# Kernel optimization log

Measured on AMD Instinct MI355X. Metric: run time of the kernel, lower is better.

Reference implementation:

```python
import jax, jax.numpy as jnp
import numpy as np

B, N, E, H, NE = 8, 512, 512, 8, 16384
DH = E // H
SCALE = DH ** -0.5
EPS = 1e-5


def _layernorm(x, g, b):
    mu = jnp.mean(x, axis=-1, keepdims=True)
    var = jnp.var(x, axis=-1, keepdims=True)
    return (x - mu) / jnp.sqrt(var + EPS) * g + b


def setup_inputs() -> dict:
    key = jax.random.key(0)
    ks = jax.random.split(key, 24)
    s = 0.02
    return {
        "x": jax.random.normal(ks[0], (B, N, E), jnp.float32),
        "edge_attr": jax.random.normal(ks[1], (NE, E), jnp.float32),
        "Wq": jax.random.normal(ks[2], (E, E), jnp.float32) * s,
        "bq": jnp.zeros((E,), jnp.float32),
        "Wk": jax.random.normal(ks[3], (E, E), jnp.float32) * s,
        "bk": jnp.zeros((E,), jnp.float32),
        "Wv": jax.random.normal(ks[4], (E, E), jnp.float32) * s,
        "bv": jnp.zeros((E,), jnp.float32),
        "Wo": jax.random.normal(ks[5], (E, E), jnp.float32) * s,
        "bo": jnp.zeros((E,), jnp.float32),
        "dist_table": jax.random.normal(ks[6], (100, H), jnp.float32),
        "We": jax.random.normal(ks[7], (H, E), jnp.float32) * s,
        "be": jnp.zeros((H,), jnp.float32),
        "W1": jax.random.normal(ks[8], (4 * E, E), jnp.float32) * s,
        "b1": jnp.zeros((4 * E,), jnp.float32),
        "W2": jax.random.normal(ks[9], (E, 4 * E), jnp.float32) * s,
        "b2": jnp.zeros((E,), jnp.float32),
        "g1": jnp.ones((E,), jnp.float32),
        "beta1": jnp.zeros((E,), jnp.float32),
        "g2": jnp.ones((E,), jnp.float32),
        "beta2": jnp.zeros((E,), jnp.float32),
        "edge_index": jax.random.randint(ks[10], (2, NE), 0, N, jnp.int64),
        "distance_matrix": jax.random.randint(ks[11], (B, N, N), 0, 100, jnp.int32),
    }


def reference(x, edge_attr, Wq, bq, Wk, bk, Wv, bv, Wo, bo, dist_table, We, be,
              W1, b1, W2, b2, g1, beta1, g2, beta2, edge_index, distance_matrix):
    residual = x
    h = _layernorm(x, g1, beta1)
    # projections -> [B, H, N, DH]
    def proj(W, b):
        return (h @ W.T + b).reshape(B, N, H, DH).transpose(0, 2, 1, 3)
    q, k, v = proj(Wq, bq), proj(Wk, bk), proj(Wv, bv)
    attn = jnp.einsum('bhnd,bhmd->bhnm', q, k) * SCALE
    # distance-encoding gather: [B,N,N] -> [B,N,N,H] -> [B,H,N,N]
    d_idx = jnp.clip(distance_matrix, 0, 99)
    attn = attn + dist_table[d_idx].transpose(0, 3, 1, 2)
    # per-edge scatter-add bias (duplicates accumulate, matching sequential loop)
    edge_enc = (edge_attr @ We.T + be).T  # [H, NE]
    src, tgt = edge_index[0], edge_index[1]
    edge_bias = jnp.zeros((H, N, N), attn.dtype).at[:, src, tgt].add(edge_enc)
    attn = attn + edge_bias[None]
    attn = jax.nn.softmax(attn, axis=-1)
    out = jnp.einsum('bhnm,bhmd->bhnd', attn, v)
    out = out.transpose(0, 2, 1, 3).reshape(B, N, E)
    out = out @ Wo.T + bo
    x1 = residual + out
    h2 = _layernorm(x1, g2, beta2)
    ffn = jax.nn.gelu(h2 @ W1.T + b1, approximate=False) @ W2.T + b2
    return x1 + ffn
```

## Files before the change

kernel.cpp:

```cpp
#include <hip/hip_runtime.h>
#include <cstdint>
#include <cstddef>

#define B_  8
#define N_  512
#define E_  512
#define H_  8
#define DH_ 64
#define NE_ 16384
#define QT  64

using u16   = unsigned short;
using bf16x8 = __attribute__((ext_vector_type(8))) __bf16;
using u16x8  = __attribute__((ext_vector_type(8))) unsigned short;
using f32x4  = __attribute__((ext_vector_type(4))) float;

__device__ __forceinline__ u16 f2b(float f) {
  unsigned u = __builtin_bit_cast(unsigned, f);
  u += 0x7fffu + ((u >> 16) & 1u);
  return (u16)(u >> 16);
}

__device__ __forceinline__ bf16x8 ld_frag(const u16* p) {
  return __builtin_bit_cast(bf16x8, *(const u16x8*)p);
}

__device__ __forceinline__ void gemm_core_128x128(
    const u16* __restrict__ At, int lda,
    const u16* __restrict__ Bt, int ldb, int K,
    u16* ldsA, u16* ldsB, f32x4 (&acc)[4][4]) {
  const int tid  = threadIdx.x;
  const int wid  = tid >> 6, lane = tid & 63;
  const int wr   = wid >> 1, wc = wid & 1;
  const int qd   = lane >> 4, r = lane & 15;
  const int mrow = tid >> 2, k0 = (tid & 3) * 8;
  for (int kt = 0; kt < K; kt += 32) {
    __syncthreads();
    *(u16x8*)&ldsA[mrow*32 + k0]      = *(const u16x8*)&At[(size_t)mrow*lda + kt + k0];
    *(u16x8*)&ldsA[(mrow+64)*32 + k0] = *(const u16x8*)&At[(size_t)(mrow+64)*lda + kt + k0];
    *(u16x8*)&ldsB[mrow*32 + k0]      = *(const u16x8*)&Bt[(size_t)mrow*ldb + kt + k0];
    *(u16x8*)&ldsB[(mrow+64)*32 + k0] = *(const u16x8*)&Bt[(size_t)(mrow+64)*ldb + kt + k0];
    __syncthreads();
    bf16x8 af[4], bfv[4];
#pragma unroll
    for (int i = 0; i < 4; ++i) af[i] = ld_frag(&ldsA[(wr*64 + i*16 + r)*32 + qd*8]);
#pragma unroll
    for (int j = 0; j < 4; ++j) bfv[j] = ld_frag(&ldsB[(wc*64 + j*16 + r)*32 + qd*8]);
#pragma unroll
    for (int i = 0; i < 4; ++i)
#pragma unroll
      for (int j = 0; j < 4; ++j)
        acc[i][j] = __builtin_amdgcn_mfma_f32_16x16x32_bf16(af[i], bfv[j], acc[i][j], 0, 0, 0);
  }
}

template <int EPI>
__global__ __launch_bounds__(256) void gemm_epi(
    const u16* __restrict__ A, const u16* __restrict__ W,
    const float* __restrict__ bias, const float* __restrict__ res,
    float* __restrict__ outf, u16* __restrict__ outb, int Kd, int Nd) {
  __shared__ u16 ldsA[128*32];
  __shared__ u16 ldsB[128*32];
  const int bx = blockIdx.x, by = blockIdx.y;
  f32x4 acc[4][4] = {};
  gemm_core_128x128(A + (size_t)bx*128*Kd, Kd, W + (size_t)by*128*Kd, Kd, Kd,
                    ldsA, ldsB, acc);
  const int tid = threadIdx.x, wid = tid>>6, lane = tid&63;
  const int wr = wid>>1, wc = wid&1, qd = lane>>4, r = lane&15;
#pragma unroll
  for (int i = 0; i < 4; ++i) {
#pragma unroll
    for (int j = 0; j < 4; ++j) {
      const int grow = bx*128 + wr*64 + i*16 + qd*4;
      const int gcol = by*128 + wc*64 + j*16 + r;
      const float bb = bias[gcol];
#pragma unroll
      for (int rg = 0; rg < 4; ++rg) {
        float v = acc[i][j][rg] + bb;
        const size_t idx = (size_t)(grow + rg)*Nd + gcol;
        if constexpr (EPI == 0) {
          outb[idx] = f2b(v);
        } else if constexpr (EPI == 1) {
          outf[idx] = v + res[idx];
        } else {
          v = 0.5f * v * (1.0f + erff(v * 0.70710678118f));
          outb[idx] = f2b(v);
        }
      }
    }
  }
}

__global__ __launch_bounds__(256) void qkv_gemm_k(
    const u16* __restrict__ A,
    const u16* __restrict__ Wqb, const u16* __restrict__ Wkb, const u16* __restrict__ Wvb,
    const float* __restrict__ bq, const float* __restrict__ bk, const float* __restrict__ bv,
    u16* __restrict__ qo, u16* __restrict__ ko, u16* __restrict__ vo) {
  __shared__ u16 ldsA[128*32];
  __shared__ u16 ldsB[128*32];
  const int bx = blockIdx.x, by = blockIdx.y, z = blockIdx.z;
  const u16*   W    = z == 0 ? Wqb : (z == 1 ? Wkb : Wvb);
  const float* bias = z == 0 ? bq  : (z == 1 ? bk  : bv);
  u16*         outb = z == 0 ? qo  : (z == 1 ? ko  : vo);
  f32x4 acc[4][4] = {};
  gemm_core_128x128(A + (size_t)bx*128*E_, E_, W + (size_t)by*128*E_, E_, E_,
                    ldsA, ldsB, acc);
  const int tid = threadIdx.x, wid = tid>>6, lane = tid&63;
  const int wr = wid>>1, wc = wid&1, qd = lane>>4, r = lane&15;
#pragma unroll
  for (int i = 0; i < 4; ++i) {
#pragma unroll
    for (int j = 0; j < 4; ++j) {
      const int grow = bx*128 + wr*64 + i*16 + qd*4;
      const int gcol = by*128 + wc*64 + j*16 + r;
      const float bb = bias[gcol];
#pragma unroll
      for (int rg = 0; rg < 4; ++rg)
        outb[(size_t)(grow + rg)*E_ + gcol] = f2b(acc[i][j][rg] + bb);
    }
  }
}

__global__ __launch_bounds__(256) void flash_attn_k(
    const u16* __restrict__ qm, const u16* __restrict__ km, const u16* __restrict__ vm,
    const float* __restrict__ dtab, const int* __restrict__ Dm,
    const float* __restrict__ ebias, u16* __restrict__ outb) {
  __shared__ u16 sQ[QT*72];
  __shared__ u16 sK[128*72];
  __shared__ u16 sP[QT*136];
  __shared__ u16 sVt[64*136];
  __shared__ float sDtab[100*H_];
  __shared__ float sMax[2][QT], sSum[2][QT], sM[QT], sL[QT], sAlpha[QT];

  const int bx = blockIdx.x;
  const int bz = blockIdx.y; const int b = bz>>3, h = bz&7;
  const int n0 = bx*QT;
  const int tid = threadIdx.x, wid = tid>>6, lane = tid&63;
  const int wr = wid>>1, wc = wid&1, qd = lane>>4, r = lane&15;

  {
    const u16* Qg = qm + ((size_t)(b*N_ + n0))*E_ + h*DH_;
#pragma unroll
    for (int it = 0; it < 2; ++it) {
      int idx = it*256 + tid;
      int row = idx>>3, d0 = (idx&7)*8;
      *(u16x8*)&sQ[row*72 + d0] = *(const u16x8*)&Qg[(size_t)row*E_ + d0];
    }
    for (int idx = tid; idx < 100*H_; idx += 256) sDtab[idx] = dtab[idx];
    if (tid < QT) { sM[tid] = -3.0e38f; sL[tid] = 0.f; }
  }

  f32x4 accO[2][2] = {};
  const int*   Db = Dm + (size_t)b*N_*N_;
  const float* Eb = ebias + (size_t)h*N_*N_;

  for (int mc = 0; mc < N_; mc += 128) {
    __syncthreads();
    {
      const u16* Kg = km + ((size_t)(b*N_ + mc))*E_ + h*DH_;
#pragma unroll
      for (int it = 0; it < 4; ++it) {
        int idx = it*256 + tid;
        int row = idx>>3, d0 = (idx&7)*8;
        *(u16x8*)&sK[row*72 + d0] = *(const u16x8*)&Kg[(size_t)row*E_ + d0];
      }
      const u16* Vg = vm + ((size_t)(b*N_ + mc))*E_ + h*DH_;
#pragma unroll
      for (int it = 0; it < 4; ++it) {
        int idx = it*256 + tid;
        int m = idx>>3, d0 = (idx&7)*8;
        u16x8 u = *(const u16x8*)&Vg[(size_t)m*E_ + d0];
#pragma unroll
        for (int e = 0; e < 8; ++e) sVt[(d0+e)*136 + m] = u[e];
      }
    }
    __syncthreads();
    f32x4 accS[2][4] = {};
#pragma unroll
    for (int ks = 0; ks < 2; ++ks) {
      bf16x8 af[2], bfv[4];
#pragma unroll
      for (int i = 0; i < 2; ++i) af[i] = ld_frag(&sQ[(wr*32 + i*16 + r)*72 + ks*32 + qd*8]);
#pragma unroll
      for (int j = 0; j < 4; ++j) bfv[j] = ld_frag(&sK[(wc*64 + j*16 + r)*72 + ks*32 + qd*8]);
#pragma unroll
      for (int i = 0; i < 2; ++i)
#pragma unroll
        for (int j = 0; j < 4; ++j)
          accS[i][j] = __builtin_amdgcn_mfma_f32_16x16x32_bf16(af[i], bfv[j], accS[i][j], 0, 0, 0);
    }
    float rmax[2][4];
#pragma unroll
    for (int i = 0; i < 2; ++i)
#pragma unroll
      for (int rg = 0; rg < 4; ++rg) rmax[i][rg] = -3.0e38f;
#pragma unroll
    for (int i = 0; i < 2; ++i) {
      const int n = n0 + wr*32 + i*16 + qd*4;
#pragma unroll
      for (int j = 0; j < 4; ++j) {
        const int m = mc + wc*64 + j*16 + r;
#pragma unroll
        for (int rg = 0; rg < 4; ++rg) {
          int di = Db[(size_t)(n+rg)*N_ + m];
          di = di < 0 ? 0 : (di > 99 ? 99 : di);
          float v = accS[i][j][rg]*0.125f + sDtab[di*H_ + h] + Eb[(size_t)(n+rg)*N_ + m];
          accS[i][j][rg] = v;
          rmax[i][rg] = fmaxf(rmax[i][rg], v);
        }
      }
    }
#pragma unroll
    for (int i = 0; i < 2; ++i)
#pragma unroll
      for (int rg = 0; rg < 4; ++rg) {
        float v = rmax[i][rg];
        v = fmaxf(v, __shfl_xor(v, 1)); v = fmaxf(v, __shfl_xor(v, 2));
        v = fmaxf(v, __shfl_xor(v, 4)); v = fmaxf(v, __shfl_xor(v, 8));
        if (r == 0) sMax[wc][wr*32 + i*16 + qd*4 + rg] = v;
      }
    __syncthreads();
    if (tid < QT) {
      float mcx  = fmaxf(sMax[0][tid], sMax[1][tid]);
      float mnew = fmaxf(sM[tid], mcx);
      sAlpha[tid] = __expf(sM[tid] - mnew);
      sM[tid] = mnew;
    }
    __syncthreads();
    float rsum[2][4];
#pragma unroll
    for (int i = 0; i < 2; ++i) {
      const int lr0 = wr*32 + i*16 + qd*4;
#pragma unroll
      for (int rg = 0; rg < 4; ++rg) {
        const float mrow = sM[lr0 + rg];
        float partial = 0.f;
#pragma unroll
        for (int j = 0; j < 4; ++j) {
          float p = __expf(accS[i][j][rg] - mrow);
          partial += p;
          sP[(lr0+rg)*136 + wc*64 + j*16 + r] = f2b(p);
        }
        rsum[i][rg] = partial;
        const float a = sAlpha[lr0 + rg];
#pragma unroll
        for (int jj = 0; jj < 2; ++jj) accO[i][jj][rg] *= a;
      }
    }
#pragma unroll
    for (int i = 0; i < 2; ++i)
#pragma unroll
      for (int rg = 0; rg < 4; ++rg) {
        float v = rsum[i][rg];
        v += __shfl_xor(v, 1); v += __shfl_xor(v, 2);
        v += __shfl_xor(v, 4); v += __shfl_xor(v, 8);
        if (r == 0) sSum[wc][wr*32 + i*16 + qd*4 + rg] = v;
      }
    __syncthreads();
    if (tid < QT) sL[tid] = sL[tid]*sAlpha[tid] + sSum[0][tid] + sSum[1][tid];
    __syncthreads();
#pragma unroll
    for (int ks = 0; ks < 4; ++ks) {
      bf16x8 af[2], bfv[2];
#pragma unroll
      for (int i = 0; i < 2; ++i) af[i] = ld_frag(&sP[(wr*32 + i*16 + r)*136 + ks*32 + qd*8]);
#pragma unroll
      for (int jj = 0; jj < 2; ++jj) bfv[jj] = ld_frag(&sVt[(wc*32 + jj*16 + r)*136 + ks*32 + qd*8]);
#pragma unroll
      for (int i = 0; i < 2; ++i)
#pragma unroll
        for (int jj = 0; jj < 2; ++jj)
          accO[i][jj] = __builtin_amdgcn_mfma_f32_16x16x32_bf16(af[i], bfv[jj], accO[i][jj], 0, 0, 0);
    }
  }
#pragma unroll
  for (int i = 0; i < 2; ++i) {
    const int lr0 = wr*32 + i*16 + qd*4;
#pragma unroll
    for (int jj = 0; jj < 2; ++jj) {
      const int d = wc*32 + jj*16 + r;
#pragma unroll
      for (int rg = 0; rg < 4; ++rg) {
        const float inv = 1.0f / sL[lr0 + rg];
        outb[((size_t)(b*N_ + n0 + lr0 + rg))*E_ + h*DH_ + d] = f2b(accO[i][jj][rg] * inv);
      }
    }
  }
}

__global__ __launch_bounds__(256) void layernorm_k(
    const float* __restrict__ x, const float* __restrict__ g,
    const float* __restrict__ be, u16* __restrict__ outb) {
  const int row = blockIdx.x, t = threadIdx.x;
  const float* xr = x + (size_t)row*E_;
  const float v0 = xr[t], v1 = xr[t+256];
  float s = v0 + v1, ss = v0*v0 + v1*v1;
  for (int o = 32; o; o >>= 1) { s += __shfl_down(s, o); ss += __shfl_down(ss, o); }
  __shared__ float rs[4], rss[4];
  const int wid = t>>6, lane = t&63;
  if (!lane) { rs[wid] = s; rss[wid] = ss; }
  __syncthreads();
  s  = rs[0]+rs[1]+rs[2]+rs[3];
  ss = rss[0]+rss[1]+rss[2]+rss[3];
  const float mu   = s * (1.0f/E_);
  const float var  = ss * (1.0f/E_) - mu*mu;
  const float rstd = rsqrtf(var + 1e-5f);
  outb[(size_t)row*E_ + t]       = f2b((v0-mu)*rstd*g[t] + be[t]);
  outb[(size_t)row*E_ + t + 256] = f2b((v1-mu)*rstd*g[t+256] + be[t+256]);
}

#define SEG0 32768
#define SEG1 65536
#define SEG2 98304
#define SEG3 131072
#define SEG4 262144
#define SEG5 393216
__global__ __launch_bounds__(256) void cvt_all_k(
    const float* __restrict__ Wq, const float* __restrict__ Wk,
    const float* __restrict__ Wv, const float* __restrict__ Wo,
    const float* __restrict__ W1, const float* __restrict__ W2,
    u16* __restrict__ wq_b, u16* __restrict__ wk_b, u16* __restrict__ wv_b,
    u16* __restrict__ wo_b, u16* __restrict__ w1_b, u16* __restrict__ w2_b) {
  const int i = blockIdx.x*256 + threadIdx.x;
  const float* src; u16* dst; int base;
  if      (i < SEG0) { src = Wq; dst = wq_b; base = 0; }
  else if (i < SEG1) { src = Wk; dst = wk_b; base = SEG0; }
  else if (i < SEG2) { src = Wv; dst = wv_b; base = SEG1; }
  else if (i < SEG3) { src = Wo; dst = wo_b; base = SEG2; }
  else if (i < SEG4) { src = W1; dst = w1_b; base = SEG3; }
  else               { src = W2; dst = w2_b; base = SEG4; }
  const int li = i - base;
  const float4 f0 = *(const float4*)&src[(size_t)li*8];
  const float4 f1 = *(const float4*)&src[(size_t)li*8 + 4];
  u16x8 u;
  u[0]=f2b(f0.x); u[1]=f2b(f0.y); u[2]=f2b(f0.z); u[3]=f2b(f0.w);
  u[4]=f2b(f1.x); u[5]=f2b(f1.y); u[6]=f2b(f1.z); u[7]=f2b(f1.w);
  *(u16x8*)&dst[(size_t)li*8] = u;
}

__global__ __launch_bounds__(256) void edge_enc_scatter_k(
    const float* __restrict__ ea, const float* __restrict__ We,
    const float* __restrict__ be, const int* __restrict__ ei,
    float* __restrict__ eb) {
  const int wglob = (blockIdx.x*256 + threadIdx.x) >> 6;
  const int lane  = threadIdx.x & 63;
  float w[8][8];
#pragma unroll
  for (int h = 0; h < 8; ++h) {
    const float4 f0 = *(const float4*)&We[h*E_ + lane*8];
    const float4 f1 = *(const float4*)&We[h*E_ + lane*8 + 4];
    w[h][0]=f0.x; w[h][1]=f0.y; w[h][2]=f0.z; w[h][3]=f0.w;
    w[h][4]=f1.x; w[h][5]=f1.y; w[h][6]=f1.z; w[h][7]=f1.w;
  }
  const float beh = (lane < 8) ? be[lane] : 0.f;
#pragma unroll 1
  for (int t = 0; t < NE_/2048; ++t) {
    const int e = wglob*(NE_/2048) + t;
    const float* ar = ea + (size_t)e*E_;
    const float4 a0 = *(const float4*)&ar[lane*8];
    const float4 a1 = *(const float4*)&ar[lane*8 + 4];
    const float a[8] = {a0.x,a0.y,a0.z,a0.w,a1.x,a1.y,a1.z,a1.w};
    float acc[8];
#pragma unroll
    for (int h = 0; h < 8; ++h) {
      float s = 0.f;
#pragma unroll
      for (int j = 0; j < 8; ++j) s += a[j]*w[h][j];
      acc[h] = s;
    }
#pragma unroll
    for (int h = 0; h < 8; ++h) {
      float v = acc[h];
      v += __shfl_xor(v, 1);  v += __shfl_xor(v, 2);  v += __shfl_xor(v, 4);
      v += __shfl_xor(v, 8);  v += __shfl_xor(v, 16); v += __shfl_xor(v, 32);
      acc[h] = v;
    }
    float myv = acc[0];
#pragma unroll
    for (int h = 1; h < 8; ++h) myv = (lane == h) ? acc[h] : myv;
    if (lane < 8) {
      const int s2 = ei[e], t2 = ei[NE_ + e];
      atomicAdd(&eb[((size_t)lane*N_ + s2)*N_ + t2], myv + beh);
    }
  }
}

extern "C" void kernel_launch(void* const* d_in, const int* in_sizes, int n_in,
                              void* d_out, int out_size, void* d_ws, size_t ws_size,
                              hipStream_t stream) {
  const float* x     = (const float*)d_in[0];
  const float* ea    = (const float*)d_in[1];
  const float* Wq    = (const float*)d_in[2];
  const float* bq    = (const float*)d_in[3];
  const float* Wk    = (const float*)d_in[4];
  const float* bk    = (const float*)d_in[5];
  const float* Wv    = (const float*)d_in[6];
  const float* bv    = (const float*)d_in[7];
  const float* Wo    = (const float*)d_in[8];
  const float* bo    = (const float*)d_in[9];
  const float* dtab  = (const float*)d_in[10];
  const float* We    = (const float*)d_in[11];
  const float* be    = (const float*)d_in[12];
  const float* W1    = (const float*)d_in[13];
  const float* b1    = (const float*)d_in[14];
  const float* W2    = (const float*)d_in[15];
  const float* b2    = (const float*)d_in[16];
  const float* g1    = (const float*)d_in[17];
  const float* bet1  = (const float*)d_in[18];
  const float* g2    = (const float*)d_in[19];
  const float* bet2  = (const float*)d_in[20];
  const int*   eidx  = (const int*)d_in[21];
  const int*   Dmat  = (const int*)d_in[22];
  float* out = (float*)d_out;

  char* ws = (char*)d_ws;
  size_t off = 0;
  auto alloc = [&](size_t bytes) -> void* {
    void* p = ws + off;
    off += (bytes + 255) & ~(size_t)255;
    return p;
  };
  u16* wq_b = (u16*)alloc((size_t)E_*E_*2);
  u16* wk_b = (u16*)alloc((size_t)E_*E_*2);
  u16* wv_b = (u16*)alloc((size_t)E_*E_*2);
  u16* wo_b = (u16*)alloc((size_t)E_*E_*2);
  u16* w1_b = (u16*)alloc((size_t)4*E_*E_*2);
  u16* w2_b = (u16*)alloc((size_t)4*E_*E_*2);
  u16* h_b  = (u16*)alloc((size_t)B_*N_*E_*2);
  u16* q_b  = (u16*)alloc((size_t)B_*N_*E_*2);
  u16* k_b  = (u16*)alloc((size_t)B_*N_*E_*2);
  u16* v_b  = (u16*)alloc((size_t)B_*N_*E_*2);
  float* ebias = (float*)alloc((size_t)H_*N_*N_*4);
  float* x1    = (float*)alloc((size_t)B_*N_*E_*4);
  u16*   h2_b  = (u16*)alloc((size_t)B_*N_*E_*2);
  u16*   mid_b = (u16*)alloc((size_t)B_*N_*4*E_*2);
  u16*   ao_b  = h_b;

  const int M = B_*N_;

  cvt_all_k<<<dim3(SEG5/256), 256, 0, stream>>>(
      Wq, Wk, Wv, Wo, W1, W2, wq_b, wk_b, wv_b, wo_b, w1_b, w2_b);

  layernorm_k<<<dim3(M), 256, 0, stream>>>(x, g1, bet1, h_b);

  qkv_gemm_k<<<dim3(M/128, E_/128, 3), 256, 0, stream>>>(
      h_b, wq_b, wk_b, wv_b, bq, bk, bv, q_b, k_b, v_b);

  hipMemsetAsync(ebias, 0, (size_t)H_*N_*N_*4, stream);
  edge_enc_scatter_k<<<dim3(512), 256, 0, stream>>>(ea, We, be, eidx, ebias);

  flash_attn_k<<<dim3(N_/QT, B_*H_), 256, 0, stream>>>(
      q_b, k_b, v_b, dtab, Dmat, ebias, ao_b);

  gemm_epi<1><<<dim3(M/128, E_/128), 256, 0, stream>>>(ao_b, wo_b, bo, x, x1, nullptr, E_, E_);

  layernorm_k<<<dim3(M), 256, 0, stream>>>(x1, g2, bet2, h2_b);

  gemm_epi<2><<<dim3(M/128, 4*E_/128), 256, 0, stream>>>(h2_b, w1_b, b1, nullptr, nullptr, mid_b, E_, 4*E_);

  gemm_epi<1><<<dim3(M/128, E_/128), 256, 0, stream>>>(mid_b, w2_b, b2, x1, out, nullptr, 4*E_, E_);
}
```

Before: 293.2 us.

## Split-K the output and FFN-down GEMMs and load GEMM tiles via direct global-to-LDS

The Wo and W2 GEMMs, which had only 128 blocks on a 256-CU device, are split along K into 2 and 4 slices that write fp32 partial sums. A separate reduce kernel then adds bias, residual and the partials. Separately, the shared GEMM core now loads its tiles with global_load_lds (16-byte direct-to-LDS) instead of going through registers. The split adds partial-buffer traffic and an extra launch, and the LDS layout from the per-wave base must match the old row-major layout the fragment reads expect.

New measurement: 280.1 us. 4.5% less time.

```diff
diff --git a/kernel.cpp b/kernel.cpp
--- a/kernel.cpp
+++ b/kernel.cpp
@@ -23,6 +23,12 @@
 
 __device__ __forceinline__ bf16x8 ld_frag(const u16* p) {
   return __builtin_bit_cast(bf16x8, *(const u16x8*)p);
+}
+
+__device__ __forceinline__ void gld_lds16(const u16* g, u16* l) {
+  __builtin_amdgcn_global_load_lds(
+      (const __attribute__((address_space(1))) unsigned*)(g),
+      (__attribute__((address_space(3))) unsigned*)(l), 16, 0, 0);
 }
 
 __device__ __forceinline__ void gemm_core_128x128(
@@ -34,12 +40,13 @@
   const int wr   = wid >> 1, wc = wid & 1;
   const int qd   = lane >> 4, r = lane & 15;
   const int mrow = tid >> 2, k0 = (tid & 3) * 8;
+  const int wbase = wid << 9;
   for (int kt = 0; kt < K; kt += 32) {
     __syncthreads();
-    *(u16x8*)&ldsA[mrow*32 + k0]      = *(const u16x8*)&At[(size_t)mrow*lda + kt + k0];
-    *(u16x8*)&ldsA[(mrow+64)*32 + k0] = *(const u16x8*)&At[(size_t)(mrow+64)*lda + kt + k0];
-    *(u16x8*)&ldsB[mrow*32 + k0]      = *(const u16x8*)&Bt[(size_t)mrow*ldb + kt + k0];
-    *(u16x8*)&ldsB[(mrow+64)*32 + k0] = *(const u16x8*)&Bt[(size_t)(mrow+64)*ldb + kt + k0];
+    gld_lds16(&At[(size_t)mrow*lda + kt + k0],        ldsA + wbase);
+    gld_lds16(&At[(size_t)(mrow+64)*lda + kt + k0],   ldsA + 64*32 + wbase);
+    gld_lds16(&Bt[(size_t)mrow*ldb + kt + k0],        ldsB + wbase);
+    gld_lds16(&Bt[(size_t)(mrow+64)*ldb + kt + k0],   ldsB + 64*32 + wbase);
     __syncthreads();
     bf16x8 af[4], bfv[4];
 #pragma unroll
@@ -89,6 +96,49 @@
       }
     }
   }
+}
+
+__global__ __launch_bounds__(256) void gemm_splitk_k(
+    const u16* __restrict__ A, const u16* __restrict__ W,
+    float* __restrict__ part, int Kd, int Nd, int Ks) {
+  __shared__ u16 ldsA[128*32];
+  __shared__ u16 ldsB[128*32];
+  const int bx = blockIdx.x, by = blockIdx.y, s = blockIdx.z;
+  f32x4 acc[4][4] = {};
+  gemm_core_128x128(A + (size_t)bx*128*Kd + (size_t)s*Ks, Kd,
+                    W + (size_t)by*128*Kd + (size_t)s*Ks, Kd, Ks,
+                    ldsA, ldsB, acc);
+  const int tid = threadIdx.x, wid = tid>>6, lane = tid&63;
+  const int wr = wid>>1, wc = wid&1, qd = lane>>4, r = lane&15;
+  float* po = part + (size_t)s*(B_*N_)*Nd;
+#pragma unroll
+  for (int i = 0; i < 4; ++i) {
+#pragma unroll
+    for (int j = 0; j < 4; ++j) {
+      const int grow = bx*128 + wr*64 + i*16 + qd*4;
+      const int gcol = by*128 + wc*64 + j*16 + r;
+#pragma unroll
+      for (int rg = 0; rg < 4; ++rg)
+        po[(size_t)(grow + rg)*Nd + gcol] = acc[i][j][rg];
+    }
+  }
+}
+
+template <int S>
+__global__ __launch_bounds__(256) void splitk_reduce_k(
+    const float* __restrict__ part, const float* __restrict__ bias,
+    const float* __restrict__ res, float* __restrict__ out) {
+  const size_t base = ((size_t)blockIdx.x*256 + threadIdx.x) * 4;
+  float4 v = *(const float4*)&res[base];
+  const int col = (int)(base & (E_-1));
+  const float4 bb = *(const float4*)&bias[col];
+  v.x += bb.x; v.y += bb.y; v.z += bb.z; v.w += bb.w;
+#pragma unroll
+  for (int s = 0; s < S; ++s) {
+    const float4 p = *(const float4*)&part[(size_t)s*(B_*N_*E_) + base];
+    v.x += p.x; v.y += p.y; v.z += p.z; v.w += p.w;
+  }
+  *(float4*)&out[base] = v;
 }
 
 __global__ __launch_bounds__(256) void qkv_gemm_k(
@@ -434,6 +484,7 @@
   float* x1    = (float*)alloc((size_t)B_*N_*E_*4);
   u16*   h2_b  = (u16*)alloc((size_t)B_*N_*E_*2);
   u16*   mid_b = (u16*)alloc((size_t)B_*N_*4*E_*2);
+  float* part  = (float*)alloc((size_t)4*B_*N_*E_*4);
   u16*   ao_b  = h_b;
 
   const int M = B_*N_;
@@ -452,11 +503,15 @@
   flash_attn_k<<<dim3(N_/QT, B_*H_), 256, 0, stream>>>(
       q_b, k_b, v_b, dtab, Dmat, ebias, ao_b);
 
-  gemm_epi<1><<<dim3(M/128, E_/128), 256, 0, stream>>>(ao_b, wo_b, bo, x, x1, nullptr, E_, E_);
+  gemm_splitk_k<<<dim3(M/128, E_/128, 2), 256, 0, stream>>>(
+      ao_b, wo_b, part, E_, E_, E_/2);
+  splitk_reduce_k<2><<<dim3(M*E_/1024), 256, 0, stream>>>(part, bo, x, x1);
 
   layernorm_k<<<dim3(M), 256, 0, stream>>>(x1, g2, bet2, h2_b);
 
   gemm_epi<2><<<dim3(M/128, 4*E_/128), 256, 0, stream>>>(h2_b, w1_b, b1, nullptr, nullptr, mid_b, E_, 4*E_);
 
-  gemm_epi<1><<<dim3(M/128, E_/128), 256, 0, stream>>>(mid_b, w2_b, b2, x1, out, nullptr, 4*E_, E_);
-}
+  gemm_splitk_k<<<dim3(M/128, E_/128, 4), 256, 0, stream>>>(
+      mid_b, w2_b, part, 4*E_, E_, E_);
+  splitk_reduce_k<4><<<dim3(M*E_/1024), 256, 0, stream>>>(part, b2, x1, out);
+}
```
